# Kernel tuning notes

Measured on AMD Instinct MI355X. Metric: run time of the kernel, lower is better.

The kernel has to match this reference:

```python
import jax, jax.numpy as jnp
import numpy as np

THRESHOLD = 1.0


def setup_inputs() -> dict:
    key = jax.random.key(0)
    ks = jax.random.split(key, 7)
    B, D = 262144, 128
    U1, U2 = 64, 32
    return {
        "x": jax.random.normal(ks[0], (B, D), dtype=jnp.float32),
        "W1": jax.random.normal(ks[1], (U1, D), dtype=jnp.float32) * 0.05,
        "b1": jax.random.normal(ks[2], (U1,), dtype=jnp.float32) * 0.05,
        "W2": jax.random.normal(ks[3], (U2, D), dtype=jnp.float32) * 0.05,
        "b2": jax.random.normal(ks[4], (U2,), dtype=jnp.float32) * 0.05,
        "Wf": jax.random.normal(ks[5], (D, U1), dtype=jnp.float32) * 0.05,
        "bf": jax.random.normal(ks[6], (D,), dtype=jnp.float32) * 0.05,
    }


def reference(x, W1, b1, W2, b2, Wf, bf):
    # Per-sample routing decision: mean |x_i| > threshold -> branch1 else branch2
    mask = jnp.mean(jnp.abs(x), axis=1) > THRESHOLD  # (B,)
    o1 = jax.nn.relu(x @ W1.T + b1)                  # (B, 64)
    o2 = jax.nn.relu(x @ W2.T + b2)                  # (B, 32)
    final_dim = W1.shape[0]                          # max(64, 32) = 64
    o2p = jnp.pad(o2, ((0, 0), (0, final_dim - o2.shape[1])))  # zero-pad to final_dim
    branch_out = jnp.where(mask[:, None], o1, o2p)   # (B, 64)
    return branch_out @ Wf.T + bf                    # (B, 128)
```

## Files before the change

### kernel.cpp

```cpp
#include <hip/hip_runtime.h>
#include <stdint.h>

#define FLAG_THRESH 127.0f

typedef short bfrag __attribute__((ext_vector_type(8)));
typedef float floatx4 __attribute__((ext_vector_type(4)));
typedef int intx4 __attribute__((ext_vector_type(4)));

__device__ __forceinline__ unsigned bf16pk(float a, float b) {
    unsigned ua = __float_as_uint(a), ub = __float_as_uint(b);
    ua = (ua + 0x7fffu + ((ua >> 16) & 1u)) >> 16;
    ub = (ub + 0x7fffu + ((ub >> 16) & 1u)) & 0xffff0000u;
    return ua | ub;
}
__device__ __forceinline__ unsigned short bf16s(float a) {
    unsigned ua = __float_as_uint(a);
    return (unsigned short)((ua + 0x7fffu + ((ua >> 16) & 1u)) >> 16);
}
__device__ __forceinline__ bfrag mkfrag(unsigned a, unsigned b, unsigned c, unsigned d) {
    intx4 v = {(int)a, (int)b, (int)c, (int)d};
    return __builtin_bit_cast(bfrag, v);
}
__device__ __forceinline__ void lds_fence_wave() {
    __builtin_amdgcn_wave_barrier();
    __builtin_amdgcn_s_waitcnt(0xc07f);
    __builtin_amdgcn_wave_barrier();
}

__global__ __launch_bounds__(256, 4)
void dyn_main(const float* __restrict__ x, const float* __restrict__ W2,
              const float* __restrict__ b2, const float* __restrict__ Wf,
              const float* __restrict__ bf, float* __restrict__ out,
              int ntiles, int* __restrict__ ws, int cap)
{
    __shared__ __align__(16) short w2f[8][64][8];
    __shared__ __align__(16) short wff[8][64][8];
    __shared__ __align__(16) float bfl[128];
    __shared__ __align__(16) short hbuf[4][16 * 40];

    const int tid  = threadIdx.x;
    const int wave = tid >> 6, lane = tid & 63;
    const int l15  = lane & 15, q = lane >> 4;

    for (int idx = tid; idx < 4096; idx += 256) {
        const int j = idx & 7, ln = (idx >> 3) & 63, blk = idx >> 9;
        const int ks = blk >> 1, nb = blk & 1;
        const int u = nb * 16 + (ln & 15);
        const int k = ks * 32 + ((ln >> 4) << 3) + j;
        ((short*)w2f)[idx] = (short)bf16s(W2[u * 128 + k]);
        const int d = blk * 16 + (ln & 15);
        const int c = ((ln >> 4) << 3) + j;
        ((short*)wff)[idx] = (short)bf16s(Wf[d * 64 + c]);
    }
    for (int i = tid; i < 128; i += 256) bfl[i] = bf[i];
    const float b2r0 = b2[l15], b2r1 = b2[16 + l15];
    __syncthreads();

    const unsigned ov = (l15 == 0) ? 0x3f803f80u : 0u;
    const bfrag onesf = mkfrag(ov, ov, ov, ov);

    const int wid = blockIdx.x * 4 + wave;
    const int wstride = gridDim.x * 4;

    long long cur = wid;
    bool more = cur < ntiles;
    floatx4 xl[8];
    if (more) {
        const float* base = x + cur * 2048 + l15 * 128 + q * 8;
        #pragma unroll
        for (int ks = 0; ks < 4; ++ks) {
            xl[2 * ks]     = *(const floatx4*)(base + ks * 32);
            xl[2 * ks + 1] = *(const floatx4*)(base + ks * 32 + 4);
        }
    }

    while (more) {
        const long long nxt = cur + wstride;
        const bool hasnxt = nxt < ntiles;
        floatx4 xc[8];
        #pragma unroll
        for (int i = 0; i < 8; ++i) xc[i] = xl[i];
        if (hasnxt) {
            const float* base = x + nxt * 2048 + l15 * 128 + q * 8;
            #pragma unroll
            for (int ks = 0; ks < 4; ++ks) {
                xl[2 * ks]     = *(const floatx4*)(base + ks * 32);
                xl[2 * ks + 1] = *(const floatx4*)(base + ks * 32 + 4);
            }
        }

        floatx4 a0 = {0.f, 0.f, 0.f, 0.f}, a1 = a0, asum = a0;
        #pragma unroll
        for (int ks = 0; ks < 4; ++ks) {
            const floatx4 p = xc[2 * ks], r = xc[2 * ks + 1];
            const unsigned u0 = bf16pk(p[0], p[1]), u1 = bf16pk(p[2], p[3]);
            const unsigned u2 = bf16pk(r[0], r[1]), u3 = bf16pk(r[2], r[3]);
            const bfrag af = mkfrag(u0, u1, u2, u3);
            const bfrag aa = mkfrag(u0 & 0x7fff7fffu, u1 & 0x7fff7fffu,
                                    u2 & 0x7fff7fffu, u3 & 0x7fff7fffu);
            const bfrag w0 = *(const bfrag*)&w2f[ks * 2 + 0][lane][0];
            const bfrag w1 = *(const bfrag*)&w2f[ks * 2 + 1][lane][0];
            a0   = __builtin_amdgcn_mfma_f32_16x16x32_bf16(af, w0, a0, 0, 0, 0);
            a1   = __builtin_amdgcn_mfma_f32_16x16x32_bf16(af, w1, a1, 0, 0, 0);
            asum = __builtin_amdgcn_mfma_f32_16x16x32_bf16(aa, onesf, asum, 0, 0, 0);
        }

        short* hb = &hbuf[wave][0];
        #pragma unroll
        for (int reg = 0; reg < 4; ++reg) {
            const int row = q * 4 + reg;
            hb[row * 40 + l15]      = (short)bf16s(fmaxf(a0[reg] + b2r0, 0.f));
            hb[row * 40 + 16 + l15] = (short)bf16s(fmaxf(a1[reg] + b2r1, 0.f));
        }

        if (l15 == 0) {
            #pragma unroll
            for (int reg = 0; reg < 4; ++reg) {
                if (asum[reg] > FLAG_THRESH) {
                    const int row = (int)(cur * 16) + q * 4 + reg;
                    const int slot = atomicAdd(ws, 1);
                    if (slot < cap) ws[4 + slot] = row;
                }
            }
        }

        lds_fence_wave();

        const bfrag hfrag = *(const bfrag*)&hb[l15 * 40 + q * 8];
        floatx4 o[8];
        #pragma unroll
        for (int mb = 0; mb < 8; ++mb) o[mb] = (floatx4){0.f, 0.f, 0.f, 0.f};
        #pragma unroll
        for (int mb = 0; mb < 8; ++mb) {
            const bfrag wfr = *(const bfrag*)&wff[mb][lane][0];
            o[mb] = __builtin_amdgcn_mfma_f32_16x16x32_bf16(wfr, hfrag, o[mb], 0, 0, 0);
        }

        float* obase = out + (cur * 16 + l15) * 128 + q * 4;
        #pragma unroll
        for (int mb = 0; mb < 8; ++mb) {
            const floatx4 bv = *(const floatx4*)&bfl[mb * 16 + q * 4];
            const floatx4 v = o[mb] + bv;
            *(floatx4*)(obase + mb * 16) = v;
        }

        lds_fence_wave();
        cur = nxt; more = hasnxt;
    }
}

__global__ __launch_bounds__(256)
void dyn_fixup(const float* __restrict__ x, const float* __restrict__ W1,
               const float* __restrict__ b1, const float* __restrict__ W2,
               const float* __restrict__ b2, const float* __restrict__ Wf,
               const float* __restrict__ bf, float* __restrict__ out,
               const int* __restrict__ ws, int cap)
{
    __shared__ float xr[4][128];
    __shared__ float hh[4][64];
    const int wave = threadIdx.x >> 6, lane = threadIdx.x & 63;
    int n = ws[0]; if (n > cap) n = cap;
    for (int i = blockIdx.x * 4 + wave; i < n; i += gridDim.x * 4) {
        const int r = ws[4 + i];
        const float2 xv = *(const float2*)&x[(long long)r * 128 + lane * 2];
        float s = fabsf(xv.x) + fabsf(xv.y);
        #pragma unroll
        for (int d = 1; d < 64; d <<= 1) s += __shfl_xor(s, d);
        xr[wave][lane * 2] = xv.x; xr[wave][lane * 2 + 1] = xv.y;
        lds_fence_wave();
        float hv = 0.f;
        if (s > 128.0f) {
            float a = 0.f;
            for (int k = 0; k < 128; k += 4) {
                const float4 qq = *(const float4*)&xr[wave][k];
                const float4 wv = *(const float4*)&W1[lane * 128 + k];
                a = fmaf(qq.x, wv.x, a); a = fmaf(qq.y, wv.y, a);
                a = fmaf(qq.z, wv.z, a); a = fmaf(qq.w, wv.w, a);
            }
            hv = fmaxf(a + b1[lane], 0.f);
        } else if (lane < 32) {
            float a = 0.f;
            for (int k = 0; k < 128; k += 4) {
                const float4 qq = *(const float4*)&xr[wave][k];
                const float4 wv = *(const float4*)&W2[lane * 128 + k];
                a = fmaf(qq.x, wv.x, a); a = fmaf(qq.y, wv.y, a);
                a = fmaf(qq.z, wv.z, a); a = fmaf(qq.w, wv.w, a);
            }
            hv = fmaxf(a + b2[lane], 0.f);
        }
        hh[wave][lane] = hv;
        lds_fence_wave();
        #pragma unroll
        for (int jj = 0; jj < 2; ++jj) {
            const int d = lane + 64 * jj;
            float a = bf[d];
            for (int u = 0; u < 64; ++u) a = fmaf(hh[wave][u], Wf[d * 64 + u], a);
            out[(long long)r * 128 + d] = a;
        }
        lds_fence_wave();
    }
}

extern "C" void kernel_launch(void* const* d_in, const int* in_sizes, int n_in,
                              void* d_out, int out_size, void* d_ws, size_t ws_size,
                              hipStream_t stream) {
    const float* x  = (const float*)d_in[0];
    const float* W1 = (const float*)d_in[1];
    const float* b1 = (const float*)d_in[2];
    const float* W2 = (const float*)d_in[3];
    const float* b2 = (const float*)d_in[4];
    const float* Wf = (const float*)d_in[5];
    const float* bf = (const float*)d_in[6];
    float* out = (float*)d_out;

    const int B = in_sizes[0] / 128;
    const int ntiles = B / 16;
    const int cap = (int)((ws_size > 16) ? ((ws_size - 16) / 4) : 0);

    hipMemsetAsync(d_ws, 0, 16, stream);
    hipLaunchKernelGGL(dyn_main, dim3(1024), dim3(256), 0, stream,
                       x, W2, b2, Wf, bf, out, ntiles, (int*)d_ws, cap);
    hipLaunchKernelGGL(dyn_fixup, dim3(64), dim3(256), 0, stream,
                       x, W1, b1, W2, b2, Wf, bf, out, (int*)d_ws, cap);
}
```

Before: 264.1 us.

## Fuse rare-row fixup into main kernel via wave ballot, drop memset and second launch

Instead of atomically appending flagged rows to a workspace list and running a separate fixup kernel, each wave builds a bitmask of flagged rows with ballots and recomputes them inline in FP32 from its own registers. Unflagged rows are stored as before, while flagged rows skip the fast-path store. This removes the memset, the atomics and the second kernel launch. In exchange the main loop gains a divergent slow path and extra LDS use, which could raise register pressure and lower occupancy.

```diff
diff --git a/kernel.cpp b/kernel.cpp
--- a/kernel.cpp
+++ b/kernel.cpp
@@ -28,15 +28,18 @@
 }
 
 __global__ __launch_bounds__(256, 4)
-void dyn_main(const float* __restrict__ x, const float* __restrict__ W2,
+void dyn_main(const float* __restrict__ x, const float* __restrict__ W1,
+              const float* __restrict__ b1, const float* __restrict__ W2,
               const float* __restrict__ b2, const float* __restrict__ Wf,
               const float* __restrict__ bf, float* __restrict__ out,
-              int ntiles, int* __restrict__ ws, int cap)
+              int ntiles)
 {
     __shared__ __align__(16) short w2f[8][64][8];
     __shared__ __align__(16) short wff[8][64][8];
     __shared__ __align__(16) float bfl[128];
     __shared__ __align__(16) short hbuf[4][16 * 40];
+    __shared__ __align__(16) float xr[4][128];
+    __shared__ __align__(16) float hh[4][64];
 
     const int tid  = threadIdx.x;
     const int wave = tid >> 6, lane = tid & 63;
@@ -105,6 +108,67 @@
             asum = __builtin_amdgcn_mfma_f32_16x16x32_bf16(aa, onesf, asum, 0, 0, 0);
         }
 
+        unsigned rowmask = 0;
+        #pragma unroll
+        for (int reg = 0; reg < 4; ++reg) {
+            const unsigned long long bm =
+                __ballot(l15 == 0 && asum[reg] > FLAG_THRESH);
+            rowmask |= (unsigned)( bm        & 1ull) << (0 + reg);
+            rowmask |= (unsigned)((bm >> 16) & 1ull) << (4 + reg);
+            rowmask |= (unsigned)((bm >> 32) & 1ull) << (8 + reg);
+            rowmask |= (unsigned)((bm >> 48) & 1ull) << (12 + reg);
+        }
+
+        if (__builtin_expect(rowmask != 0, 0)) {
+            unsigned m = rowmask;
+            while (m) {
+                const int r = (int)__builtin_ctz(m); m &= m - 1;
+                if (l15 == r) {
+                    #pragma unroll
+                    for (int ks = 0; ks < 4; ++ks) {
+                        *(floatx4*)&xr[wave][ks * 32 + q * 8]     = xc[2 * ks];
+                        *(floatx4*)&xr[wave][ks * 32 + q * 8 + 4] = xc[2 * ks + 1];
+                    }
+                }
+                lds_fence_wave();
+                const float e0 = xr[wave][lane * 2], e1 = xr[wave][lane * 2 + 1];
+                float s = fabsf(e0) + fabsf(e1);
+                #pragma unroll
+                for (int d = 1; d < 64; d <<= 1) s += __shfl_xor(s, d);
+                float hv = 0.f;
+                if (s > 128.0f) {
+                    float a = 0.f;
+                    for (int k = 0; k < 128; k += 4) {
+                        const float4 qq = *(const float4*)&xr[wave][k];
+                        const float4 wv = *(const float4*)&W1[lane * 128 + k];
+                        a = fmaf(qq.x, wv.x, a); a = fmaf(qq.y, wv.y, a);
+                        a = fmaf(qq.z, wv.z, a); a = fmaf(qq.w, wv.w, a);
+                    }
+                    hv = fmaxf(a + b1[lane], 0.f);
+                } else if (lane < 32) {
+                    float a = 0.f;
+                    for (int k = 0; k < 128; k += 4) {
+                        const float4 qq = *(const float4*)&xr[wave][k];
+                        const float4 wv = *(const float4*)&W2[lane * 128 + k];
+                        a = fmaf(qq.x, wv.x, a); a = fmaf(qq.y, wv.y, a);
+                        a = fmaf(qq.z, wv.z, a); a = fmaf(qq.w, wv.w, a);
+                    }
+                    hv = fmaxf(a + b2[lane], 0.f);
+                }
+                hh[wave][lane] = hv;
+                lds_fence_wave();
+                #pragma unroll
+                for (int jj = 0; jj < 2; ++jj) {
+                    const int d = lane + 64 * jj;
+                    float a = bf[d];
+                    for (int u = 0; u < 64; ++u)
+                        a = fmaf(hh[wave][u], Wf[d * 64 + u], a);
+                    out[(cur * 16 + r) * 128 + d] = a;
+                }
+                lds_fence_wave();
+            }
+        }
+
         short* hb = &hbuf[wave][0];
         #pragma unroll
         for (int reg = 0; reg < 4; ++reg) {
@@ -113,17 +177,6 @@
             hb[row * 40 + 16 + l15] = (short)bf16s(fmaxf(a1[reg] + b2r1, 0.f));
         }
 
-        if (l15 == 0) {
-            #pragma unroll
-            for (int reg = 0; reg < 4; ++reg) {
-                if (asum[reg] > FLAG_THRESH) {
-                    const int row = (int)(cur * 16) + q * 4 + reg;
-                    const int slot = atomicAdd(ws, 1);
-                    if (slot < cap) ws[4 + slot] = row;
-                }
-            }
-        }
-
         lds_fence_wave();
 
         const bfrag hfrag = *(const bfrag*)&hb[l15 * 40 + q * 8];
@@ -137,67 +190,26 @@
         }
 
         float* obase = out + (cur * 16 + l15) * 128 + q * 4;
-        #pragma unroll
-        for (int mb = 0; mb < 8; ++mb) {
-            const floatx4 bv = *(const floatx4*)&bfl[mb * 16 + q * 4];
-            const floatx4 v = o[mb] + bv;
-            *(floatx4*)(obase + mb * 16) = v;
+        if (__builtin_expect(rowmask == 0, 1)) {
+            #pragma unroll
+            for (int mb = 0; mb < 8; ++mb) {
+                const floatx4 bv = *(const floatx4*)&bfl[mb * 16 + q * 4];
+                const floatx4 v = o[mb] + bv;
+                *(floatx4*)(obase + mb * 16) = v;
+            }
+        } else {
+            if (((rowmask >> l15) & 1u) == 0u) {
+                #pragma unroll
+                for (int mb = 0; mb < 8; ++mb) {
+                    const floatx4 bv = *(const floatx4*)&bfl[mb * 16 + q * 4];
+                    const floatx4 v = o[mb] + bv;
+                    *(floatx4*)(obase + mb * 16) = v;
+                }
+            }
         }
 
         lds_fence_wave();
         cur = nxt; more = hasnxt;
-    }
-}
-
-__global__ __launch_bounds__(256)
-void dyn_fixup(const float* __restrict__ x, const float* __restrict__ W1,
-               const float* __restrict__ b1, const float* __restrict__ W2,
-               const float* __restrict__ b2, const float* __restrict__ Wf,
-               const float* __restrict__ bf, float* __restrict__ out,
-               const int* __restrict__ ws, int cap)
-{
-    __shared__ float xr[4][128];
-    __shared__ float hh[4][64];
-    const int wave = threadIdx.x >> 6, lane = threadIdx.x & 63;
-    int n = ws[0]; if (n > cap) n = cap;
-    for (int i = blockIdx.x * 4 + wave; i < n; i += gridDim.x * 4) {
-        const int r = ws[4 + i];
-        const float2 xv = *(const float2*)&x[(long long)r * 128 + lane * 2];
-        float s = fabsf(xv.x) + fabsf(xv.y);
-        #pragma unroll
-        for (int d = 1; d < 64; d <<= 1) s += __shfl_xor(s, d);
-        xr[wave][lane * 2] = xv.x; xr[wave][lane * 2 + 1] = xv.y;
-        lds_fence_wave();
-        float hv = 0.f;
-        if (s > 128.0f) {
-            float a = 0.f;
-            for (int k = 0; k < 128; k += 4) {
-                const float4 qq = *(const float4*)&xr[wave][k];
-                const float4 wv = *(const float4*)&W1[lane * 128 + k];
-                a = fmaf(qq.x, wv.x, a); a = fmaf(qq.y, wv.y, a);
-                a = fmaf(qq.z, wv.z, a); a = fmaf(qq.w, wv.w, a);
-            }
-            hv = fmaxf(a + b1[lane], 0.f);
-        } else if (lane < 32) {
-            float a = 0.f;
-            for (int k = 0; k < 128; k += 4) {
-                const float4 qq = *(const float4*)&xr[wave][k];
-                const float4 wv = *(const float4*)&W2[lane * 128 + k];
-                a = fmaf(qq.x, wv.x, a); a = fmaf(qq.y, wv.y, a);
-                a = fmaf(qq.z, wv.z, a); a = fmaf(qq.w, wv.w, a);
-            }
-            hv = fmaxf(a + b2[lane], 0.f);
-        }
-        hh[wave][lane] = hv;
-        lds_fence_wave();
-        #pragma unroll
-        for (int jj = 0; jj < 2; ++jj) {
-            const int d = lane + 64 * jj;
-            float a = bf[d];
-            for (int u = 0; u < 64; ++u) a = fmaf(hh[wave][u], Wf[d * 64 + u], a);
-            out[(long long)r * 128 + d] = a;
-        }
-        lds_fence_wave();
     }
 }
 
@@ -212,14 +224,11 @@
     const float* Wf = (const float*)d_in[5];
     const float* bf = (const float*)d_in[6];
     float* out = (float*)d_out;
+    (void)d_ws; (void)ws_size;
 
     const int B = in_sizes[0] / 128;
     const int ntiles = B / 16;
-    const int cap = (int)((ws_size > 16) ? ((ws_size - 16) / 4) : 0);
-
-    hipMemsetAsync(d_ws, 0, 16, stream);
+
     hipLaunchKernelGGL(dyn_main, dim3(1024), dim3(256), 0, stream,
-                       x, W2, b2, Wf, bf, out, ntiles, (int*)d_ws, cap);
-    hipLaunchKernelGGL(dyn_fixup, dim3(64), dim3(256), 0, stream,
-                       x, W1, b1, W2, b2, Wf, bf, out, (int*)d_ws, cap);
-}
+                       x, W1, b1, W2, b2, Wf, bf, out, ntiles);
+}
```

New measurement: 262.2 us. Within noise of the previous version (-0.7%).
